# Kernel tuning notes

Hardware: AMD Instinct MI355X
Metric: run time of the kernel (lower is better)

The kernel has to match this reference:

```python
import jax, jax.numpy as jnp
import numpy as np

D_EMBED = 1024
N_HEADS = 16


def setup_inputs() -> dict:
    key = jax.random.key(0)
    ks = jax.random.split(key, 5)
    x = jax.random.normal(ks[0], (4, 2048, D_EMBED), dtype=jnp.float32)
    # fused QKV projection: Linear(d, 3d)
    w_qkv = jax.random.normal(ks[1], (D_EMBED, 3 * D_EMBED), dtype=jnp.float32) / np.sqrt(D_EMBED)
    b_qkv = jnp.zeros((3 * D_EMBED,), dtype=jnp.float32)
    # output projection: Linear(d, d)
    w_o = jax.random.normal(ks[2], (D_EMBED, D_EMBED), dtype=jnp.float32) / np.sqrt(D_EMBED)
    b_o = jnp.zeros((D_EMBED,), dtype=jnp.float32)
    return {"x": x, "w_qkv": w_qkv, "b_qkv": b_qkv, "w_o": w_o, "b_o": b_o}


def reference(x, w_qkv, b_qkv, w_o, b_o):
    bs, sl, ed = x.shape
    nh = N_HEADS
    hd = ed // nh
    qkv = x @ w_qkv + b_qkv                      # [bs, sl, 3*ed]
    q, k, v = jnp.split(qkv, 3, axis=-1)
    # (bs, sl, nh*hd) -> (bs, nh, sl, hd)
    q = q.reshape(bs, sl, nh, hd).transpose(0, 2, 1, 3)
    k = k.reshape(bs, sl, nh, hd).transpose(0, 2, 1, 3)
    v = v.reshape(bs, sl, nh, hd).transpose(0, 2, 1, 3)
    att = jnp.einsum('bhqd,bhkd->bhqk', q, k) * (1.0 / np.sqrt(hd))
    causal = jnp.tril(jnp.ones((sl, sl), dtype=bool))
    att = jnp.where(causal[None, None], att, jnp.float32(-jnp.inf))
    att = jax.nn.softmax(att, axis=-1)
    y = jnp.einsum('bhqk,bhkd->bhqd', att, v)    # [bs, nh, sl, hd]
    y = y.transpose(0, 2, 1, 3).reshape(bs, sl, ed)
    return y @ w_o + b_o
```

## Files before the change

### kernel.cpp

```cpp
#include <hip/hip_runtime.h>
#include <hip/hip_bf16.h>
#include <stdint.h>

typedef __attribute__((ext_vector_type(8))) __bf16 bf16x8;
typedef __attribute__((ext_vector_type(4))) __bf16 bf16x4;
typedef __attribute__((ext_vector_type(4))) float f32x4;

#define MFMA16(a, b, c) __builtin_amdgcn_mfma_f32_16x16x32_bf16((a), (b), (c), 0, 0, 0)

static __device__ __forceinline__ void gload_lds16(const void* g, void* l) {
  __builtin_amdgcn_global_load_lds(
      reinterpret_cast<const __attribute__((address_space(1))) uint32_t*>(
          reinterpret_cast<uintptr_t>(g)),
      reinterpret_cast<__attribute__((address_space(3))) uint32_t*>(
          reinterpret_cast<uintptr_t>(l)),
      16, 0, 0);
}

__global__ __launch_bounds__(256) void prep_fused(
    const float* __restrict__ x, __bf16* __restrict__ xb,
    const float* __restrict__ wqkv, __bf16* __restrict__ wqkvT,
    const float* __restrict__ wo, __bf16* __restrict__ woT) {
  __shared__ float tile[32][33];
  const int bid = (int)blockIdx.x;
  const int tid = threadIdx.x;
  if (bid < 4096) {
    int i = bid * 2048 + tid * 8;
    float4 a = *(const float4*)(x + i);
    float4 b = *(const float4*)(x + i + 4);
    bf16x8 o;
    o[0] = (__bf16)a.x; o[1] = (__bf16)a.y; o[2] = (__bf16)a.z; o[3] = (__bf16)a.w;
    o[4] = (__bf16)b.x; o[5] = (__bf16)b.y; o[6] = (__bf16)b.z; o[7] = (__bf16)b.w;
    *(bf16x8*)(xb + i) = o;
    return;
  }
  const float* in;
  __bf16* out;
  int C, bx, by;
  if (bid < 7168) {
    int t = bid - 4096;
    in = wqkv; out = wqkvT; C = 3072;
    bx = t % 96; by = t / 96;
  } else {
    int t = bid - 7168;
    in = wo; out = woT; C = 1024;
    bx = t & 31; by = t >> 5;
  }
  const int R = 1024;
  int tx = tid & 31, ty = tid >> 5;
  int c0 = bx * 32, r0 = by * 32;
#pragma unroll
  for (int i = 0; i < 4; i++)
    tile[ty + i * 8][tx] = in[(size_t)(r0 + ty + i * 8) * C + c0 + tx];
  __syncthreads();
#pragma unroll
  for (int i = 0; i < 4; i++)
    out[(size_t)(c0 + ty + i * 8) * R + r0 + tx] = (__bf16)tile[tx][ty + i * 8];
}

template <int EPI, int NPAN>
__global__ __launch_bounds__(512) void gemm_pipe(
    const __bf16* __restrict__ A, const __bf16* __restrict__ Bt,
    const float* __restrict__ bias, float* __restrict__ Cf,
    __bf16* __restrict__ Qb, __bf16* __restrict__ Kb, __bf16* __restrict__ Vtb, int N) {
  __shared__ __bf16 lA[3][128 * 32];
  __shared__ __bf16 lB[3][256 * 32];
  const int bid0 = (int)blockIdx.x;
  const int tM = (bid0 & 7) * 8 + ((bid0 >> 3) & 7);
  const int tN0 = bid0 >> 6;
  const int tid = threadIdx.x;
  const int w = tid >> 6, lane = tid & 63;
  const int wr = w >> 2, wc = w & 3;
  const int lr = lane & 15, lg = lane >> 4;

  const int srow = tid >> 2;
  const int gcol = ((tid & 3) ^ ((tid >> 3) & 3)) * 8;
  const __bf16* Asrc = A + (size_t)(tM * 128 + srow) * 1024 + gcol;
  const int aslot = (lg ^ ((lr >> 1) & 3)) * 8;

#pragma unroll 1
  for (int p = 0; p < NPAN; ++p) {
    const int tN = tN0 + p * 4;
    const __bf16* Bsrc0 = Bt + (size_t)(tN * 256 + srow) * 1024 + gcol;
    const __bf16* Bsrc1 = Bt + (size_t)(tN * 256 + 128 + srow) * 1024 + gcol;

    f32x4 acc[4][4];
#pragma unroll
    for (int m = 0; m < 4; m++)
#pragma unroll
      for (int n = 0; n < 4; n++) acc[m][n] = f32x4{0.f, 0.f, 0.f, 0.f};

    auto stage = [&](int slot, int t) {
      const int k0 = t * 32;
      gload_lds16(Asrc + k0, &lA[slot][tid * 8]);
      gload_lds16(Bsrc0 + k0, &lB[slot][tid * 8]);
      gload_lds16(Bsrc1 + k0, &lB[slot][4096 + tid * 8]);
    };
    auto compute = [&](int slot) {
      bf16x8 a[4], b[4];
#pragma unroll
      for (int m = 0; m < 4; m++) {
        int row = wr * 64 + m * 16 + lr;
        a[m] = *(const bf16x8*)&lA[slot][row * 32 + aslot];
      }
#pragma unroll
      for (int n = 0; n < 4; n++) {
        int row = wc * 64 + n * 16 + lr;
        b[n] = *(const bf16x8*)&lB[slot][row * 32 + aslot];
      }
      __builtin_amdgcn_s_setprio(1);
#pragma unroll
      for (int m = 0; m < 4; m++)
#pragma unroll
        for (int n = 0; n < 4; n++) acc[m][n] = MFMA16(a[m], b[n], acc[m][n]);
      __builtin_amdgcn_s_setprio(0);
    };

    stage(0, 0); stage(1, 1);
    asm volatile("s_waitcnt vmcnt(3)" ::: "memory");
    __builtin_amdgcn_s_barrier();

#pragma unroll 1
    for (int t = 0; t < 30; ++t) {
      stage((t + 2) % 3, t + 2);
      compute(t % 3);
      asm volatile("s_waitcnt vmcnt(3)" ::: "memory");
      __builtin_amdgcn_s_barrier();
    }
    compute(30 % 3);
    asm volatile("s_waitcnt vmcnt(0)" ::: "memory");
    __builtin_amdgcn_s_barrier();
    compute(31 % 3);

#pragma unroll
    for (int m = 0; m < 4; m++) {
#pragma unroll
      for (int n = 0; n < 4; n++) {
        int row0 = tM * 128 + wr * 64 + m * 16 + lg * 4;
        int col = tN * 256 + wc * 64 + n * 16 + lr;
        float bv = bias[col];
        if (EPI == 0) {
          int which = col >> 10, rem = col & 1023;
          int hh = rem >> 6, dd = rem & 63;
          if (which == 2) {
#pragma unroll
            for (int r = 0; r < 4; r++) {
              int row = row0 + r;
              int b = row >> 11, s = row & 2047;
              Vtb[((size_t)(b * 16 + hh) * 64 + dd) * 2048 + s] = (__bf16)(acc[m][n][r] + bv);
            }
          } else {
            __bf16* dst = (which == 0) ? Qb : Kb;
            float sc = (which == 0) ? 0.18033688f : 1.0f;
#pragma unroll
            for (int r = 0; r < 4; r++) {
              int row = row0 + r;
              int b = row >> 11, s = row & 2047;
              dst[((size_t)(b * 16 + hh) * 2048 + s) * 64 + dd] = (__bf16)((acc[m][n][r] + bv) * sc);
            }
          }
        } else {
#pragma unroll
          for (int r = 0; r < 4; r++)
            Cf[(size_t)(row0 + r) * N + col] = acc[m][n][r] + bv;
        }
      }
    }
    if (p + 1 < NPAN) __syncthreads();
  }
}

__global__ __launch_bounds__(256) void attn_fwd(
    const __bf16* __restrict__ Q, const __bf16* __restrict__ K,
    const __bf16* __restrict__ Vt, __bf16* __restrict__ Y) {
  const int pair = blockIdx.y;
  const int bh = blockIdx.x;
  const int w = threadIdx.x >> 6, lane = threadIdx.x & 63;
  const int lr = lane & 15, lg = lane >> 4;
  const int b = bh >> 4, h = bh & 15;
  const __bf16* Qp = Q + (size_t)bh * 131072;
  const __bf16* Kp = K + (size_t)bh * 131072;
  const __bf16* Vp = Vt + (size_t)bh * 131072;

  __shared__ __bf16 Kl[4][4096];
  __shared__ __bf16 Vl[4][4096];
  __shared__ __bf16 Pl[4][32 * 64];
  __bf16* Pw = Pl[w];

  bf16x8 kones;
#pragma unroll
  for (int j = 0; j < 8; j++) kones[j] = (__bf16)1.0f;

  auto stage = [&](int slot, int t_) {
    const int kv0_ = t_ * 64;
#pragma unroll
    for (int is = 0; is < 2; is++) {
      int rr = w * 16 + is * 8 + (lane >> 3);
      int sc = ((lane & 7) ^ (rr & 7)) * 8;
      gload_lds16(Kp + (size_t)(kv0_ + rr) * 64 + sc, &Kl[slot][(w * 16 + is * 8) * 64]);
      gload_lds16(Vp + (size_t)rr * 2048 + kv0_ + sc, &Vl[slot][(w * 16 + is * 8) * 64]);
    }
  };

  for (int sel = 0; sel < 2; ++sel) {
    const int qt = sel ? (15 - pair) : pair;
    const int qbase = qt * 128 + w * 32;

    bf16x8 aq[2][2];
#pragma unroll
    for (int m = 0; m < 2; m++)
#pragma unroll
      for (int c = 0; c < 2; c++)
        aq[m][c] = *(const bf16x8*)&Qp[(size_t)(qbase + m * 16 + lr) * 64 + c * 32 + lg * 8];

    f32x4 acc_o[2][4];
    f32x4 acc_l[2];
#pragma unroll
    for (int m = 0; m < 2; m++) {
#pragma unroll
      for (int dn = 0; dn < 4; dn++) acc_o[m][dn] = f32x4{0.f, 0.f, 0.f, 0.f};
      acc_l[m] = f32x4{0.f, 0.f, 0.f, 0.f};
    }

    const int nt = 2 * qt + 2;

    stage(0, 0);
    stage(1, 1);

#pragma unroll 1
    for (int t = 0; t < nt; ++t) {
      const int kv0 = t * 64;
      if (t + 2 < nt) stage((t + 2) & 3, t + 2);

      if (t + 2 < nt) {
        asm volatile("s_waitcnt vmcnt(8)" ::: "memory");
      } else if (t + 1 < nt) {
        asm volatile("s_waitcnt vmcnt(4)" ::: "memory");
      } else {
        asm volatile("s_waitcnt vmcnt(0)" ::: "memory");
      }
      __builtin_amdgcn_s_barrier();

      if (kv0 <= qbase + 31) {
        const int cur = t & 3;
        f32x4 s4[2][4];
#pragma unroll
        for (int m = 0; m < 2; m++)
#pragma unroll
          for (int n = 0; n < 4; n++) s4[m][n] = f32x4{0.f, 0.f, 0.f, 0.f};
        __builtin_amdgcn_s_setprio(1);
#pragma unroll
        for (int c = 0; c < 2; c++) {
#pragma unroll
          for (int n = 0; n < 4; n++) {
            int kr = n * 16 + lr;
            int off = kr * 64 + (((c * 64 + lg * 16) ^ ((kr & 7) << 4)) >> 1);
            bf16x8 bk = *(const bf16x8*)&Kl[cur][off];
#pragma unroll
            for (int m = 0; m < 2; m++) s4[m][n] = MFMA16(bk, aq[m][c], s4[m][n]);
          }
        }
        __builtin_amdgcn_s_setprio(0);

        const bool diag = (kv0 + 63 > qbase);
#pragma unroll
        for (int m = 0; m < 2; m++) {
          const int qrow = qbase + m * 16 + lr;
          if (diag) {
#pragma unroll
            for (int n = 0; n < 4; n++)
#pragma unroll
              for (int r = 0; r < 4; r++)
                if (kv0 + n * 16 + lg * 4 + r > qrow) s4[m][n][r] = -1e30f;
          }
#pragma unroll
          for (int n = 0; n < 4; n++) {
            bf16x4 pq;
#pragma unroll
            for (int r = 0; r < 4; r++)
              pq[r] = (__bf16)__builtin_amdgcn_exp2f(s4[m][n][r] - 16.0f);
            int off = (m * 16 + lr) * 64 + (((n * 32 + lg * 8) ^ ((lr & 7) << 4)) >> 1);
            *(bf16x4*)&Pw[off] = pq;
          }
        }

        bf16x8 ap[2][2];
#pragma unroll
        for (int m = 0; m < 2; m++)
#pragma unroll
          for (int cc = 0; cc < 2; cc++) {
            int off = (m * 16 + lr) * 64 + (((cc * 64 + lg * 16) ^ ((lr & 7) << 4)) >> 1);
            ap[m][cc] = *(const bf16x8*)&Pw[off];
          }

        __builtin_amdgcn_s_setprio(1);
#pragma unroll
        for (int m = 0; m < 2; m++)
#pragma unroll
          for (int cc = 0; cc < 2; cc++)
            acc_l[m] = MFMA16(ap[m][cc], kones, acc_l[m]);
#pragma unroll
        for (int dn = 0; dn < 4; dn++) {
          int d = dn * 16 + lr;
#pragma unroll
          for (int cc = 0; cc < 2; cc++) {
            int off = d * 64 + (((cc * 64 + lg * 16) ^ ((d & 7) << 4)) >> 1);
            bf16x8 bv = *(const bf16x8*)&Vl[cur][off];
#pragma unroll
            for (int m = 0; m < 2; m++) acc_o[m][dn] = MFMA16(ap[m][cc], bv, acc_o[m][dn]);
          }
        }
        __builtin_amdgcn_s_setprio(0);
      }
    }

    __syncthreads();

#pragma unroll
    for (int m = 0; m < 2; m++) {
#pragma unroll
      for (int r = 0; r < 4; r++) {
        float iv = 1.f / acc_l[m][r];
        int row = b * 2048 + qbase + m * 16 + lg * 4 + r;
#pragma unroll
        for (int dn = 0; dn < 4; dn++)
          Y[(size_t)row * 1024 + h * 64 + dn * 16 + lr] = (__bf16)(acc_o[m][dn][r] * iv);
      }
    }
  }
}

extern "C" void kernel_launch(void* const* d_in, const int* in_sizes, int n_in,
                              void* d_out, int out_size, void* d_ws, size_t ws_size,
                              hipStream_t stream) {
  const float* x = (const float*)d_in[0];
  const float* wqkv = (const float*)d_in[1];
  const float* bqkv = (const float*)d_in[2];
  const float* wo = (const float*)d_in[3];
  const float* bo = (const float*)d_in[4];
  float* out = (float*)d_out;

  __bf16* ws = (__bf16*)d_ws;
  __bf16* xb = ws;
  __bf16* wqkvT = xb + 8388608;
  __bf16* woT = wqkvT + 3145728;
  __bf16* Qb = woT + 1048576;
  __bf16* Kb = Qb + 8388608;
  __bf16* Vtb = Kb + 8388608;
  __bf16* Yb = xb;

  prep_fused<<<8192, 256, 0, stream>>>(x, xb, wqkv, wqkvT, wo, woT);
  gemm_pipe<0, 3><<<256, 512, 0, stream>>>(xb, wqkvT, bqkv, nullptr, Qb, Kb, Vtb, 3072);
  attn_fwd<<<dim3(64, 8), 256, 0, stream>>>(Qb, Kb, Vtb, Yb);
  gemm_pipe<1, 1><<<256, 512, 0, stream>>>(Yb, woT, bo, out, nullptr, nullptr, nullptr, 1024);
}
```

Measured before the change: 157.7 us.

## Split attention block across 8 waves with 16 query rows each

The attention kernel now launches 512 threads per block instead of 256. Each wave handles 16 query rows instead of 32, and K/V staging is spread over 8 waves with adjusted vmcnt waits. The aim is more waves per CU to hide latency, plus finer causal skipping per wave. The trade-off is that each loaded K/V fragment feeds half as many MFMAs, so more LDS reads are needed per unit of compute.

New measurement: 146.8 us (median of 2 runs). 6.9% less time.

```diff
diff --git a/kernel.cpp b/kernel.cpp
--- a/kernel.cpp
+++ b/kernel.cpp
@@ -170,7 +170,7 @@
   }
 }
 
-__global__ __launch_bounds__(256) void attn_fwd(
+__global__ __launch_bounds__(512) void attn_fwd(
     const __bf16* __restrict__ Q, const __bf16* __restrict__ K,
     const __bf16* __restrict__ Vt, __bf16* __restrict__ Y) {
   const int pair = blockIdx.y;
@@ -184,7 +184,7 @@
 
   __shared__ __bf16 Kl[4][4096];
   __shared__ __bf16 Vl[4][4096];
-  __shared__ __bf16 Pl[4][32 * 64];
+  __shared__ __bf16 Pl[8][16 * 64];
   __bf16* Pw = Pl[w];
 
   bf16x8 kones;
@@ -193,34 +193,26 @@
 
   auto stage = [&](int slot, int t_) {
     const int kv0_ = t_ * 64;
-#pragma unroll
-    for (int is = 0; is < 2; is++) {
-      int rr = w * 16 + is * 8 + (lane >> 3);
-      int sc = ((lane & 7) ^ (rr & 7)) * 8;
-      gload_lds16(Kp + (size_t)(kv0_ + rr) * 64 + sc, &Kl[slot][(w * 16 + is * 8) * 64]);
-      gload_lds16(Vp + (size_t)rr * 2048 + kv0_ + sc, &Vl[slot][(w * 16 + is * 8) * 64]);
-    }
+    int rr = w * 8 + (lane >> 3);
+    int sc = ((lane & 7) ^ (rr & 7)) * 8;
+    gload_lds16(Kp + (size_t)(kv0_ + rr) * 64 + sc, &Kl[slot][w * 512]);
+    gload_lds16(Vp + (size_t)rr * 2048 + kv0_ + sc, &Vl[slot][w * 512]);
   };
 
   for (int sel = 0; sel < 2; ++sel) {
     const int qt = sel ? (15 - pair) : pair;
-    const int qbase = qt * 128 + w * 32;
-
-    bf16x8 aq[2][2];
-#pragma unroll
-    for (int m = 0; m < 2; m++)
-#pragma unroll
-      for (int c = 0; c < 2; c++)
-        aq[m][c] = *(const bf16x8*)&Qp[(size_t)(qbase + m * 16 + lr) * 64 + c * 32 + lg * 8];
-
-    f32x4 acc_o[2][4];
-    f32x4 acc_l[2];
-#pragma unroll
-    for (int m = 0; m < 2; m++) {
-#pragma unroll
-      for (int dn = 0; dn < 4; dn++) acc_o[m][dn] = f32x4{0.f, 0.f, 0.f, 0.f};
-      acc_l[m] = f32x4{0.f, 0.f, 0.f, 0.f};
-    }
+    const int qbase = qt * 128 + w * 16;
+
+    bf16x8 aq[2];
+#pragma unroll
+    for (int c = 0; c < 2; c++)
+      aq[c] = *(const bf16x8*)&Qp[(size_t)(qbase + lr) * 64 + c * 32 + lg * 8];
+
+    f32x4 acc_o[4];
+    f32x4 acc_l;
+#pragma unroll
+    for (int dn = 0; dn < 4; dn++) acc_o[dn] = f32x4{0.f, 0.f, 0.f, 0.f};
+    acc_l = f32x4{0.f, 0.f, 0.f, 0.f};
 
     const int nt = 2 * qt + 2;
 
@@ -233,21 +225,19 @@
       if (t + 2 < nt) stage((t + 2) & 3, t + 2);
 
       if (t + 2 < nt) {
-        asm volatile("s_waitcnt vmcnt(8)" ::: "memory");
+        asm volatile("s_waitcnt vmcnt(4)" ::: "memory");
       } else if (t + 1 < nt) {
-        asm volatile("s_waitcnt vmcnt(4)" ::: "memory");
+        asm volatile("s_waitcnt vmcnt(2)" ::: "memory");
       } else {
         asm volatile("s_waitcnt vmcnt(0)" ::: "memory");
       }
       __builtin_amdgcn_s_barrier();
 
-      if (kv0 <= qbase + 31) {
+      if (kv0 <= qbase + 15) {
         const int cur = t & 3;
-        f32x4 s4[2][4];
-#pragma unroll
-        for (int m = 0; m < 2; m++)
-#pragma unroll
-          for (int n = 0; n < 4; n++) s4[m][n] = f32x4{0.f, 0.f, 0.f, 0.f};
+        f32x4 s4[4];
+#pragma unroll
+        for (int n = 0; n < 4; n++) s4[n] = f32x4{0.f, 0.f, 0.f, 0.f};
         __builtin_amdgcn_s_setprio(1);
 #pragma unroll
         for (int c = 0; c < 2; c++) {
@@ -256,49 +246,41 @@
             int kr = n * 16 + lr;
             int off = kr * 64 + (((c * 64 + lg * 16) ^ ((kr & 7) << 4)) >> 1);
             bf16x8 bk = *(const bf16x8*)&Kl[cur][off];
-#pragma unroll
-            for (int m = 0; m < 2; m++) s4[m][n] = MFMA16(bk, aq[m][c], s4[m][n]);
+            s4[n] = MFMA16(bk, aq[c], s4[n]);
           }
         }
         __builtin_amdgcn_s_setprio(0);
 
         const bool diag = (kv0 + 63 > qbase);
-#pragma unroll
-        for (int m = 0; m < 2; m++) {
-          const int qrow = qbase + m * 16 + lr;
-          if (diag) {
-#pragma unroll
-            for (int n = 0; n < 4; n++)
-#pragma unroll
-              for (int r = 0; r < 4; r++)
-                if (kv0 + n * 16 + lg * 4 + r > qrow) s4[m][n][r] = -1e30f;
-          }
-#pragma unroll
-          for (int n = 0; n < 4; n++) {
-            bf16x4 pq;
+        const int qrow = qbase + lr;
+        if (diag) {
+#pragma unroll
+          for (int n = 0; n < 4; n++)
 #pragma unroll
             for (int r = 0; r < 4; r++)
-              pq[r] = (__bf16)__builtin_amdgcn_exp2f(s4[m][n][r] - 16.0f);
-            int off = (m * 16 + lr) * 64 + (((n * 32 + lg * 8) ^ ((lr & 7) << 4)) >> 1);
-            *(bf16x4*)&Pw[off] = pq;
-          }
-        }
-
-        bf16x8 ap[2][2];
-#pragma unroll
-        for (int m = 0; m < 2; m++)
-#pragma unroll
-          for (int cc = 0; cc < 2; cc++) {
-            int off = (m * 16 + lr) * 64 + (((cc * 64 + lg * 16) ^ ((lr & 7) << 4)) >> 1);
-            ap[m][cc] = *(const bf16x8*)&Pw[off];
-          }
+              if (kv0 + n * 16 + lg * 4 + r > qrow) s4[n][r] = -1e30f;
+        }
+#pragma unroll
+        for (int n = 0; n < 4; n++) {
+          bf16x4 pq;
+#pragma unroll
+          for (int r = 0; r < 4; r++)
+            pq[r] = (__bf16)__builtin_amdgcn_exp2f(s4[n][r] - 16.0f);
+          int off = lr * 64 + (((n * 32 + lg * 8) ^ ((lr & 7) << 4)) >> 1);
+          *(bf16x4*)&Pw[off] = pq;
+        }
+
+        bf16x8 ap[2];
+#pragma unroll
+        for (int cc = 0; cc < 2; cc++) {
+          int off = lr * 64 + (((cc * 64 + lg * 16) ^ ((lr & 7) << 4)) >> 1);
+          ap[cc] = *(const bf16x8*)&Pw[off];
+        }
 
         __builtin_amdgcn_s_setprio(1);
 #pragma unroll
-        for (int m = 0; m < 2; m++)
-#pragma unroll
-          for (int cc = 0; cc < 2; cc++)
-            acc_l[m] = MFMA16(ap[m][cc], kones, acc_l[m]);
+        for (int cc = 0; cc < 2; cc++)
+          acc_l = MFMA16(ap[cc], kones, acc_l);
 #pragma unroll
         for (int dn = 0; dn < 4; dn++) {
           int d = dn * 16 + lr;
@@ -306,8 +288,7 @@
           for (int cc = 0; cc < 2; cc++) {
             int off = d * 64 + (((cc * 64 + lg * 16) ^ ((d & 7) << 4)) >> 1);
             bf16x8 bv = *(const bf16x8*)&Vl[cur][off];
-#pragma unroll
-            for (int m = 0; m < 2; m++) acc_o[m][dn] = MFMA16(ap[m][cc], bv, acc_o[m][dn]);
+            acc_o[dn] = MFMA16(ap[cc], bv, acc_o[dn]);
           }
         }
         __builtin_amdgcn_s_setprio(0);
@@ -317,15 +298,12 @@
     __syncthreads();
 
 #pragma unroll
-    for (int m = 0; m < 2; m++) {
-#pragma unroll
-      for (int r = 0; r < 4; r++) {
-        float iv = 1.f / acc_l[m][r];
-        int row = b * 2048 + qbase + m * 16 + lg * 4 + r;
-#pragma unroll
-        for (int dn = 0; dn < 4; dn++)
-          Y[(size_t)row * 1024 + h * 64 + dn * 16 + lr] = (__bf16)(acc_o[m][dn][r] * iv);
-      }
+    for (int r = 0; r < 4; r++) {
+      float iv = 1.f / acc_l[r];
+      int row = b * 2048 + qbase + lg * 4 + r;
+#pragma unroll
+      for (int dn = 0; dn < 4; dn++)
+        Y[(size_t)row * 1024 + h * 64 + dn * 16 + lr] = (__bf16)(acc_o[dn][r] * iv);
     }
   }
 }
@@ -351,6 +329,6 @@
 
   prep_fused<<<8192, 256, 0, stream>>>(x, xb, wqkv, wqkvT, wo, woT);
   gemm_pipe<0, 3><<<256, 512, 0, stream>>>(xb, wqkvT, bqkv, nullptr, Qb, Kb, Vtb, 3072);
-  attn_fwd<<<dim3(64, 8), 256, 0, stream>>>(Qb, Kb, Vtb, Yb);
+  attn_fwd<<<dim3(64, 8), 512, 0, stream>>>(Qb, Kb, Vtb, Yb);
   gemm_pipe<1, 1><<<256, 512, 0, stream>>>(Yb, woT, bo, out, nullptr, nullptr, nullptr, 1024);
 }
```
